# Kernel optimization log

Measured on AMD Instinct MI355X. Metric: run time of the kernel, lower is better.

Reference implementation:

```python
import jax, jax.numpy as jnp
import numpy as np
import math

NEG = -1000000.0


def setup_inputs() -> dict:
    key = jax.random.key(0)
    ks = jax.random.split(key, 8)
    B, S, D = 4, 2048, 1024
    std = 1.0 / math.sqrt(D)
    return {
        "queries": jax.random.normal(ks[0], (B, S, D), jnp.float32),
        "keys": jax.random.normal(ks[1], (B, S, D), jnp.float32),
        "values": jax.random.normal(ks[2], (B, S, D), jnp.float32),
        "valid_len": jax.random.randint(ks[3], (B,), 1, S, dtype=jnp.int64 if jax.config.jax_enable_x64 else jnp.int32),
        "W_q": jax.random.normal(ks[4], (D, D), jnp.float32) * std,
        "W_k": jax.random.normal(ks[5], (D, D), jnp.float32) * std,
        "W_v": jax.random.normal(ks[6], (D, D), jnp.float32) * std,
        "W_o": jax.random.normal(ks[7], (D, D), jnp.float32) * std,
    }


def reference(queries, keys, values, valid_len, W_q, W_k, W_v, W_o):
    NUM_HEADS = 16
    B, S, D = queries.shape
    hd = D // NUM_HEADS

    def split_heads(x):
        # (B, S, D) -> (B, H, S, hd)
        return x.reshape(B, -1, NUM_HEADS, hd).transpose(0, 2, 1, 3)

    # nn.Linear with weight W applies x @ W.T
    q = split_heads(queries @ W_q.T)
    k = split_heads(keys @ W_k.T)
    v = split_heads(values @ W_v.T)

    scale = 1.0 / math.sqrt(hd)
    scores = jnp.einsum('bhqd,bhkd->bhqk', q, k) * scale  # (B, H, Sq, Sk)

    # key-padding mask from valid_len: positions >= valid_len are masked
    kpos = jnp.arange(scores.shape[-1])
    pad_mask = kpos[None, None, None, :] >= valid_len[:, None, None, None]
    scores = jnp.where(pad_mask, NEG, scores)
    attn = jax.nn.softmax(scores, axis=-1)

    out = jnp.einsum('bhqk,bhkd->bhqd', attn, v)  # (B, H, Sq, hd)
    out = out.transpose(0, 2, 1, 3).reshape(B, -1, D)
    return out @ W_o.T
```

## Files before the change

kernel.cpp:

```cpp
#include <hip/hip_runtime.h>
#include <hip/hip_bf16.h>

using bf16_t = __bf16;
using bf16x8 = __attribute__((ext_vector_type(8))) __bf16;
using bf16x4 = __attribute__((ext_vector_type(4))) __bf16;
using f32x4  = __attribute__((ext_vector_type(4))) float;

#define S_  2048
#define D_  1024

typedef __attribute__((address_space(1))) unsigned int glb_u32;
typedef __attribute__((address_space(3))) unsigned int lds_u32;

__device__ __forceinline__ void async_cp16(const void* g, void* lds) {
    __builtin_amdgcn_global_load_lds(
        (glb_u32*)(unsigned long long)g,
        (lds_u32*)(unsigned int)(unsigned long long)lds,
        16, 0, 0);
}

__global__ __launch_bounds__(256) void cast4_f32_bf16(const float* __restrict__ a, const float* __restrict__ b,
                                                      const float* __restrict__ c, const float* __restrict__ dd,
                                                      bf16_t* __restrict__ oa, bf16_t* __restrict__ ob,
                                                      bf16_t* __restrict__ oc, bf16_t* __restrict__ od, int n4) {
    int i = blockIdx.x * 256 + threadIdx.x;
    if (i >= n4) return;
    const float* s; bf16_t* d;
    int w = blockIdx.y;
    if      (w == 0) { s = a;  d = oa; }
    else if (w == 1) { s = b;  d = ob; }
    else if (w == 2) { s = c;  d = oc; }
    else             { s = dd; d = od; }
    float4 f = reinterpret_cast<const float4*>(s)[i];
    bf16x4 o;
    o[0] = (bf16_t)f.x; o[1] = (bf16_t)f.y; o[2] = (bf16_t)f.z; o[3] = (bf16_t)f.w;
    reinterpret_cast<bf16x4*>(d)[i] = o;
}

__global__ __launch_bounds__(256) void cast3_f32_bf16(const float* __restrict__ q, const float* __restrict__ k,
                                                      const float* __restrict__ v,
                                                      bf16_t* __restrict__ oq, bf16_t* __restrict__ ok,
                                                      bf16_t* __restrict__ ov, int n4) {
    int i = blockIdx.x * 256 + threadIdx.x;
    if (i >= n4) return;
    const float* s; bf16_t* d;
    int w = blockIdx.y;
    if      (w == 0) { s = q; d = oq; }
    else if (w == 1) { s = k; d = ok; }
    else             { s = v; d = ov; }
    float4 f = reinterpret_cast<const float4*>(s)[i];
    bf16x4 o;
    o[0] = (bf16_t)f.x; o[1] = (bf16_t)f.y; o[2] = (bf16_t)f.z; o[3] = (bf16_t)f.w;
    reinterpret_cast<bf16x4*>(d)[i] = o;
}

template <int MODE>
__global__ __launch_bounds__(512, 2) void gemm8(const bf16_t* __restrict__ Aq,
                                                const bf16_t* __restrict__ Ak,
                                                const bf16_t* __restrict__ Av,
                                                const bf16_t* __restrict__ Wq,
                                                const bf16_t* __restrict__ Wk,
                                                const bf16_t* __restrict__ Wv,
                                                bf16_t* __restrict__ Qp,
                                                bf16_t* __restrict__ Kp,
                                                bf16_t* __restrict__ Vt,
                                                float cs,
                                                float* __restrict__ Co) {
    __shared__ bf16_t As[2][2][256 * 32];
    __shared__ bf16_t Bs[2][2][256 * 32];
    const int K = 1024;
    constexpr int NKT = 16;
    int tid  = threadIdx.x;
    int lane = tid & 63, w = tid >> 6;
    int l15  = lane & 15, quad = lane >> 4;
    int wr = w >> 2, wc = w & 3;

    int bid = blockIdx.x;
    int xcd = bid & 7, r = bid >> 3;
    int z = 0, r2 = r;
    if (MODE == 0) { z = r >> 4; r2 = r & 15; }
    int m0 = (xcd * 4 + (r2 & 3)) * 256;
    int n0 = (r2 >> 2) * 256;

    const bf16_t *Ag, *Bg;
    if (MODE == 0) {
        Ag = (z == 0) ? Aq : (z == 1) ? Ak : Av;
        Bg = (z == 0) ? Wq : (z == 1) ? Wk : Wv;
    } else { Ag = Aq; Bg = Wq; }

    const bf16_t* aS[2]; const bf16_t* bS[2]; int ldOff[2];
#pragma unroll
    for (int j = 0; j < 2; j++) {
        int c = j * 512 + tid;
        int row = c >> 2, s = c & 3;
        int ks = (s ^ ((row >> 1) & 3)) * 8;
        aS[j] = Ag + (size_t)(m0 + row) * K + ks;
        bS[j] = Bg + (size_t)(n0 + row) * K + ks;
        ldOff[j] = c * 8;
    }
    auto stage = [&](int buf, int t, int half) {
        int kh = half >> 1;
        int koff = t * 64 + kh * 32;
        if ((half & 1) == 0) {
            async_cp16(aS[0] + koff, &As[buf][kh][ldOff[0]]);
            async_cp16(aS[1] + koff, &As[buf][kh][ldOff[1]]);
        } else {
            async_cp16(bS[0] + koff, &Bs[buf][kh][ldOff[0]]);
            async_cp16(bS[1] + koff, &Bs[buf][kh][ldOff[1]]);
        }
    };

    int aoff[8], boff[4];
#pragma unroll
    for (int i = 0; i < 8; i++) {
        int row = wr * 128 + i * 16 + l15;
        aoff[i] = row * 32 + ((quad ^ ((row >> 1) & 3)) * 8);
    }
#pragma unroll
    for (int jn = 0; jn < 4; jn++) {
        int row = wc * 64 + jn * 16 + l15;
        boff[jn] = row * 32 + ((quad ^ ((row >> 1) & 3)) * 8);
    }

    f32x4 acc[8][4] = {};

    stage(0, 0, 0); stage(0, 0, 1); stage(0, 0, 2); stage(0, 0, 3);
    asm volatile("s_waitcnt vmcnt(4)" ::: "memory");
    __builtin_amdgcn_s_barrier();

    for (int t = 0; t < NKT; ++t) {
        int buf = t & 1, nbuf = buf ^ 1;
        bool st = (t + 1 < NKT);
        const bf16_t* A0 = As[buf][0]; const bf16_t* A1 = As[buf][1];
        const bf16_t* B0 = Bs[buf][0]; const bf16_t* B1 = Bs[buf][1];
        bf16x8 af[4], bfr[4];

#pragma unroll
        for (int i = 0; i < 4; i++) af[i] = *reinterpret_cast<const bf16x8*>(&A0[aoff[i]]);
#pragma unroll
        for (int jn = 0; jn < 4; jn++) bfr[jn] = *reinterpret_cast<const bf16x8*>(&B0[boff[jn]]);
        if (st) stage(nbuf, t + 1, 0);
        __builtin_amdgcn_s_barrier();
        asm volatile("s_waitcnt lgkmcnt(0)" ::: "memory");
        __builtin_amdgcn_sched_barrier(0);
        __builtin_amdgcn_s_setprio(1);
#pragma unroll
        for (int i = 0; i < 4; i++)
#pragma unroll
            for (int jn = 0; jn < 4; jn++)
                acc[i][jn] = __builtin_amdgcn_mfma_f32_16x16x32_bf16(af[i], bfr[jn], acc[i][jn], 0, 0, 0);
        __builtin_amdgcn_s_setprio(0);
        __builtin_amdgcn_s_barrier();

#pragma unroll
        for (int i = 0; i < 4; i++) af[i] = *reinterpret_cast<const bf16x8*>(&A0[aoff[4 + i]]);
        if (st) stage(nbuf, t + 1, 1);
        __builtin_amdgcn_s_barrier();
        asm volatile("s_waitcnt lgkmcnt(0)" ::: "memory");
        __builtin_amdgcn_sched_barrier(0);
        __builtin_amdgcn_s_setprio(1);
#pragma unroll
        for (int i = 0; i < 4; i++)
#pragma unroll
            for (int jn = 0; jn < 4; jn++)
                acc[4 + i][jn] = __builtin_amdgcn_mfma_f32_16x16x32_bf16(af[i], bfr[jn], acc[4 + i][jn], 0, 0, 0);
        __builtin_amdgcn_s_setprio(0);
        if (t == NKT - 1) asm volatile("s_waitcnt vmcnt(0)" ::: "memory");
        else              asm volatile("s_waitcnt vmcnt(4)" ::: "memory");
        __builtin_amdgcn_s_barrier();

#pragma unroll
        for (int i = 0; i < 4; i++) af[i] = *reinterpret_cast<const bf16x8*>(&A1[aoff[i]]);
#pragma unroll
        for (int jn = 0; jn < 4; jn++) bfr[jn] = *reinterpret_cast<const bf16x8*>(&B1[boff[jn]]);
        if (st) stage(nbuf, t + 1, 2);
        __builtin_amdgcn_s_barrier();
        asm volatile("s_waitcnt lgkmcnt(0)" ::: "memory");
        __builtin_amdgcn_sched_barrier(0);
        __builtin_amdgcn_s_setprio(1);
#pragma unroll
        for (int i = 0; i < 4; i++)
#pragma unroll
            for (int jn = 0; jn < 4; jn++)
                acc[i][jn] = __builtin_amdgcn_mfma_f32_16x16x32_bf16(af[i], bfr[jn], acc[i][jn], 0, 0, 0);
        __builtin_amdgcn_s_setprio(0);
        __builtin_amdgcn_s_barrier();

#pragma unroll
        for (int i = 0; i < 4; i++) af[i] = *reinterpret_cast<const bf16x8*>(&A1[aoff[4 + i]]);
        if (st) stage(nbuf, t + 1, 3);
        __builtin_amdgcn_s_barrier();
        asm volatile("s_waitcnt lgkmcnt(0)" ::: "memory");
        __builtin_amdgcn_sched_barrier(0);
        __builtin_amdgcn_s_setprio(1);
#pragma unroll
        for (int i = 0; i < 4; i++)
#pragma unroll
            for (int jn = 0; jn < 4; jn++)
                acc[4 + i][jn] = __builtin_amdgcn_mfma_f32_16x16x32_bf16(af[i], bfr[jn], acc[4 + i][jn], 0, 0, 0);
        __builtin_amdgcn_s_setprio(0);
        asm volatile("s_waitcnt vmcnt(4)" ::: "memory");
        __builtin_amdgcn_s_barrier();
    }

    if (MODE == 0 && z == 2) {
#pragma unroll
        for (int i = 0; i < 8; i++)
#pragma unroll
            for (int jn = 0; jn < 4; jn++) {
                int m = m0 + wr * 128 + i * 16 + quad * 4;
                int n = n0 + wc * 64 + jn * 16 + l15;
                bf16x4 o4;
#pragma unroll
                for (int rr = 0; rr < 4; rr++) o4[rr] = (bf16_t)acc[i][jn][rr];
                size_t vrow = (size_t)((m >> 11) * 16 + (n >> 6)) * 64 + (n & 63);
                int ml = m & 2047;
                int mp = (ml & ~31) | (((ml >> 2) & 3) << 3) | (((ml >> 4) & 1) << 2);
                *reinterpret_cast<bf16x4*>(&Vt[vrow * S_ + mp]) = o4;
            }
    } else if (MODE == 0) {
        bf16_t* CoH = (z == 0) ? Qp : Kp;
        float scale = (z == 0) ? cs : 1.0f;
#pragma unroll
        for (int i = 0; i < 8; i++)
#pragma unroll
            for (int jn = 0; jn < 4; jn++)
#pragma unroll
                for (int rr = 0; rr < 4; rr++) {
                    int m = m0 + wr * 128 + i * 16 + quad * 4 + rr;
                    int n = n0 + wc * 64 + jn * 16 + l15;
                    CoH[(size_t)m * 1024 + n] = (bf16_t)(acc[i][jn][rr] * scale);
                }
    } else {
#pragma unroll
        for (int i = 0; i < 8; i++)
#pragma unroll
            for (int jn = 0; jn < 4; jn++)
#pragma unroll
                for (int rr = 0; rr < 4; rr++) {
                    int m = m0 + wr * 128 + i * 16 + quad * 4 + rr;
                    int n = n0 + wc * 64 + jn * 16 + l15;
                    Co[(size_t)m * 1024 + n] = acc[i][jn][rr];
                }
    }
}

__global__ __launch_bounds__(256, 4) void qkv_gemm(const float* __restrict__ qf,
                                                   const float* __restrict__ kf,
                                                   const float* __restrict__ vf,
                                                   const bf16_t* __restrict__ Wqb,
                                                   const bf16_t* __restrict__ Wkb,
                                                   const bf16_t* __restrict__ Wvb,
                                                   bf16_t* __restrict__ Qp,
                                                   bf16_t* __restrict__ Kp,
                                                   bf16_t* __restrict__ Vt,
                                                   float cs) {
    __shared__ bf16_t As[2][128 * 32];
    __shared__ bf16_t Bs[3][128 * 32];
    const int K = 1024;
    int tid  = threadIdx.x;
    int lane = tid & 63;
    int w    = tid >> 6;
    int l15  = lane & 15, quad = lane >> 4;

    int bid = blockIdx.x;
    int xcd = bid & 7, idx = bid >> 3;
    int z   = idx >> 6;
    int rem = idx & 63;
    int m0 = (xcd * 8 + (rem & 7)) * 128;
    int n0 = (rem >> 3) * 128;
    int wm = (w >> 1) * 64, wn = (w & 1) * 64;

    const float*  Af; const bf16_t* Bt;
    if      (z == 0) { Af = qf; Bt = Wqb; }
    else if (z == 1) { Af = kf; Bt = Wkb; }
    else             { Af = vf; Bt = Wvb; }
    float scale = (z == 0) ? cs : 1.0f;

    const float* Ag = Af + (size_t)(m0 + (tid >> 2)) * K + (tid & 3) * 8;
    int arow = tid >> 2, aslot = tid & 3;
    int aoff = arow * 32 + ((aslot ^ ((arow >> 1) & 3)) * 8);

    const bf16_t* bSrc[2]; int bOff[2];
#pragma unroll
    for (int j = 0; j < 2; j++) {
        int linear = j * 256 + tid;
        int row = linear >> 2, s = linear & 3;
        bSrc[j] = Bt + (size_t)(n0 + row) * K + ((s ^ ((row >> 1) & 3)) * 8);
        bOff[j] = linear * 8;
    }

    float4 aE[4], aO[4];
    auto loadA = [&](float4* a, int k0) {
        const float* p = Ag + k0;
        a[0] = *reinterpret_cast<const float4*>(p);
        a[1] = *reinterpret_cast<const float4*>(p + 4);
        a[2] = *reinterpret_cast<const float4*>(p + (size_t)64 * K);
        a[3] = *reinterpret_cast<const float4*>(p + (size_t)64 * K + 4);
    };
    auto storeA = [&](bf16_t* dst, const float4* a) {
        bf16x8 o0, o1;
        o0[0] = (bf16_t)a[0].x; o0[1] = (bf16_t)a[0].y; o0[2] = (bf16_t)a[0].z; o0[3] = (bf16_t)a[0].w;
        o0[4] = (bf16_t)a[1].x; o0[5] = (bf16_t)a[1].y; o0[6] = (bf16_t)a[1].z; o0[7] = (bf16_t)a[1].w;
        o1[0] = (bf16_t)a[2].x; o1[1] = (bf16_t)a[2].y; o1[2] = (bf16_t)a[2].z; o1[3] = (bf16_t)a[2].w;
        o1[4] = (bf16_t)a[3].x; o1[5] = (bf16_t)a[3].y; o1[6] = (bf16_t)a[3].z; o1[7] = (bf16_t)a[3].w;
        *reinterpret_cast<bf16x8*>(dst + aoff)        = o0;
        *reinterpret_cast<bf16x8*>(dst + aoff + 2048) = o1;
    };
    auto stageB = [&](bf16_t* dst, int k0) {
        async_cp16(bSrc[0] + k0, dst + bOff[0]);
        async_cp16(bSrc[1] + k0, dst + bOff[1]);
    };

    f32x4 acc[4][4] = {};
    bf16_t *bRead = Bs[0], *bMid = Bs[1], *bStage = Bs[2];

    loadA(aE, 0);
    stageB(Bs[0], 0);
    loadA(aO, 32);
    stageB(Bs[1], 32);
    storeA(As[0], aE);
    asm volatile("s_waitcnt vmcnt(6) lgkmcnt(0)" ::: "memory");
    __builtin_amdgcn_s_barrier();

#pragma unroll 2
    for (int i = 0; i < 32; ++i) {
        int k2 = (i + 2 < 32) ? (i + 2) * 32 : 992;
        float4* aNew = (i & 1) ? aO : aE;
        loadA(aNew, k2);
        stageB(bStage, k2);

        const bf16_t* Ac = As[i & 1];
        bf16x8 af[4], bfr[4];
#pragma unroll
        for (int t = 0; t < 4; t++) {
            int ra = wm + t * 16 + l15;
            int rb = wn + t * 16 + l15;
            af[t]  = *reinterpret_cast<const bf16x8*>(&Ac[ra * 32 + ((quad ^ ((ra >> 1) & 3)) * 8)]);
            bfr[t] = *reinterpret_cast<const bf16x8*>(&bRead[rb * 32 + ((quad ^ ((rb >> 1) & 3)) * 8)]);
        }
#pragma unroll
        for (int mt = 0; mt < 4; mt++)
#pragma unroll
            for (int nt = 0; nt < 4; nt++)
                acc[mt][nt] = __builtin_amdgcn_mfma_f32_16x16x32_bf16(af[mt], bfr[nt], acc[mt][nt], 0, 0, 0);

        if (i + 1 < 32) storeA(As[(i + 1) & 1], (i & 1) ? aE : aO);

        bf16_t* t0 = bRead; bRead = bMid; bMid = bStage; bStage = t0;
        asm volatile("s_waitcnt vmcnt(6) lgkmcnt(0)" ::: "memory");
        __builtin_amdgcn_s_barrier();
    }

    if (z == 2) {
#pragma unroll
        for (int mt = 0; mt < 4; mt++)
#pragma unroll
            for (int nt = 0; nt < 4; nt++) {
                int m = m0 + wm + mt * 16 + quad * 4;
                int n = n0 + wn + nt * 16 + l15;
                bf16x4 o4;
#pragma unroll
                for (int r = 0; r < 4; r++) o4[r] = (bf16_t)acc[mt][nt][r];
                size_t vrow = (size_t)((m >> 11) * 16 + (n >> 6)) * 64 + (n & 63);
                int ml = m & 2047;
                int mp = (ml & ~31) | (((ml >> 2) & 3) << 3) | (((ml >> 4) & 1) << 2);
                *reinterpret_cast<bf16x4*>(&Vt[vrow * S_ + mp]) = o4;
            }
    } else {
        bf16_t* Co = (z == 0) ? Qp : Kp;
#pragma unroll
        for (int mt = 0; mt < 4; mt++)
#pragma unroll
            for (int nt = 0; nt < 4; nt++)
#pragma unroll
                for (int r = 0; r < 4; r++) {
                    int m = m0 + wm + mt * 16 + quad * 4 + r;
                    int n = n0 + wn + nt * 16 + l15;
                    Co[(size_t)m * 1024 + n] = (bf16_t)(acc[mt][nt][r] * scale);
                }
    }
}

__global__ __launch_bounds__(256) void attn_fused(const bf16_t* __restrict__ Qp,
                                                  const bf16_t* __restrict__ Kp,
                                                  const bf16_t* __restrict__ Vt,
                                                  const int* __restrict__ vlen_p,
                                                  bf16_t* __restrict__ Out) {
    __shared__ bf16_t smem[4][64 * 64];

    int tid  = threadIdx.x;
    int lane = tid & 63, w = tid >> 6;
    int l15  = lane & 15, quad = lane >> 4;

    int nk[4], ord[4] = {0, 1, 2, 3};
#pragma unroll
    for (int i = 0; i < 4; i++) nk[i] = (vlen_p[i] + 63) >> 6;
#pragma unroll
    for (int i = 0; i < 3; i++)
#pragma unroll
        for (int j = 0; j < 3 - i; j++)
            if (nk[ord[j + 1]] > nk[ord[j]]) { int t = ord[j]; ord[j] = ord[j + 1]; ord[j + 1] = t; }

    int bid  = blockIdx.x;
    int b    = ord[bid >> 9];
    int t    = bid & 511;
    int h    = (t & 7) * 2 + ((t >> 3) & 1);
    int qblk = t >> 4;
    int vlen = vlen_p[b];
    int nkb  = (vlen + 63) >> 6;

    const bf16_t* Qg = Qp + (size_t)(b * S_ + qblk * 64) * D_ + h * 64;
    const bf16_t* Kg = Kp + (size_t)b * S_ * D_ + h * 64;
    const bf16_t* Vg = Vt + (size_t)(b * 16 + h) * 64 * S_;

    int r0 = tid >> 3, s0 = tid & 7;
    int sx = (s0 ^ (r0 & 7)) * 8;
    const bf16_t* kS0 = Kg + (size_t)r0 * D_ + sx;
    const bf16_t* kS1 = kS0 + (size_t)32 * D_;
    const bf16_t* vS0 = Vg + (size_t)r0 * S_ + sx;
    const bf16_t* vS1 = vS0 + (size_t)32 * S_;

    {
        const bf16_t* qS0 = Qg + (size_t)r0 * D_ + sx;
        async_cp16(qS0,                   smem[2] + tid * 8);
        async_cp16(qS0 + (size_t)32 * D_, smem[2] + tid * 8 + 2048);
        async_cp16(kS0, smem[0] + tid * 8);
        async_cp16(kS1, smem[0] + tid * 8 + 2048);
        async_cp16(vS0, smem[1] + tid * 8);
        async_cp16(vS1, smem[1] + tid * 8 + 2048);
    }
    __syncthreads();

    bf16x8 qf[2];
    {
        int row = w * 16 + l15, x = row & 7;
#pragma unroll
        for (int kk = 0; kk < 2; kk++)
            qf[kk] = *reinterpret_cast<const bf16x8*>(&smem[2][row * 64 + ((kk * 4 + quad) ^ x) * 8]);
    }
    __syncthreads();

    f32x4 o[4] = {};
    float l_st = 0.f;

    for (int kb = 0; kb < nkb; kb++) {
        int cur = kb & 1;
        if (kb + 1 < nkb) {
            int nxt = cur ^ 1;
            kS0 += (size_t)64 * D_; kS1 += (size_t)64 * D_;
            vS0 += 64;              vS1 += 64;
            async_cp16(kS0, smem[nxt * 2]     + tid * 8);
            async_cp16(kS1, smem[nxt * 2]     + tid * 8 + 2048);
            async_cp16(vS0, smem[nxt * 2 + 1] + tid * 8);
            async_cp16(vS1, smem[nxt * 2 + 1] + tid * 8 + 2048);
        }
        const bf16_t* Kc = smem[cur * 2];
        const bf16_t* Vc = smem[cur * 2 + 1];

        f32x4 sc[4] = {};
#pragma unroll
        for (int nt = 0; nt < 4; nt++) {
            int row = nt * 16 + l15, x = row & 7;
#pragma unroll
            for (int kk = 0; kk < 2; kk++) {
                bf16x8 kf = *reinterpret_cast<const bf16x8*>(&Kc[row * 64 + ((kk * 4 + quad) ^ x) * 8]);
                sc[nt] = __builtin_amdgcn_mfma_f32_16x16x32_bf16(kf, qf[kk], sc[nt], 0, 0, 0);
            }
        }

        bool partial = (vlen & 63) && (kb == nkb - 1);
        bf16x8 pf[2];
        float lacc = 0.f;
        if (!partial) {
#pragma unroll
            for (int nt = 0; nt < 4; nt++)
#pragma unroll
                for (int r = 0; r < 4; r++) {
                    float p = __builtin_exp2f(sc[nt][r]);
                    lacc += p;
                    pf[nt >> 1][(nt & 1) * 4 + r] = (bf16_t)p;
                }
        } else {
#pragma unroll
            for (int nt = 0; nt < 4; nt++)
#pragma unroll
                for (int r = 0; r < 4; r++) {
                    float p = __builtin_exp2f(sc[nt][r]);
                    if (kb * 64 + nt * 16 + quad * 4 + r >= vlen) p = 0.f;
                    lacc += p;
                    pf[nt >> 1][(nt & 1) * 4 + r] = (bf16_t)p;
                }
        }
        l_st += lacc;

#pragma unroll
        for (int np = 0; np < 2; np++)
#pragma unroll
            for (int dt = 0; dt < 4; dt++) {
                int row = dt * 16 + l15, x = row & 7;
                bf16x8 vfr = *reinterpret_cast<const bf16x8*>(&Vc[row * 64 + ((np * 4 + quad) ^ x) * 8]);
                o[dt] = __builtin_amdgcn_mfma_f32_16x16x32_bf16(vfr, pf[np], o[dt], 0, 0, 0);
            }

        __syncthreads();
    }

    float l = l_st;
    l += __shfl_xor(l, 16);
    l += __shfl_xor(l, 32);
    float inv = 1.0f / l;

    bf16_t* T = smem[0];
    {
        int row = w * 16 + l15, x = row & 7;
#pragma unroll
        for (int dt = 0; dt < 4; dt++) {
            bf16x4 o4;
#pragma unroll
            for (int r = 0; r < 4; r++) o4[r] = (bf16_t)(o[dt][r] * inv);
            int slot = dt * 2 + (quad >> 1);
            *reinterpret_cast<bf16x4*>(&T[row * 64 + (slot ^ x) * 8 + (quad & 1) * 4]) = o4;
        }
    }
    __syncthreads();
    {
        int row = tid >> 2, ch = tid & 3, x = row & 7;
        size_t obase = (size_t)(b * S_ + qblk * 64 + row) * D_ + h * 64 + ch * 16;
        bf16x8 f0 = *reinterpret_cast<const bf16x8*>(&T[row * 64 + ((ch * 2)     ^ x) * 8]);
        bf16x8 f1 = *reinterpret_cast<const bf16x8*>(&T[row * 64 + ((ch * 2 + 1) ^ x) * 8]);
        *reinterpret_cast<bf16x8*>(&Out[obase])     = f0;
        *reinterpret_cast<bf16x8*>(&Out[obase + 8]) = f1;
    }
}

__global__ __launch_bounds__(256) void gemm_out(const bf16_t* __restrict__ A,
                                                const bf16_t* __restrict__ Bt,
                                                float* __restrict__ C) {
    __shared__ bf16_t As[3][128 * 32];
    __shared__ bf16_t Bs[3][128 * 32];
    const int K = 1024;
    int tid  = threadIdx.x;
    int lane = tid & 63;
    int w    = tid >> 6;
    int l15  = lane & 15, quad = lane >> 4;

    int bid = blockIdx.x;
    int xcd = bid & 7, idx = bid >> 3;
    int m0 = (xcd * 8 + (idx & 7)) * 128;
    int n0 = (idx >> 3) * 128;
    int wm = (w >> 1) * 64, wn = (w & 1) * 64;

    const bf16_t* aSrc[2]; const bf16_t* bSrc[2];
    int dOff[2];
#pragma unroll
    for (int j = 0; j < 2; j++) {
        int linear = j * 256 + tid;
        int row = linear >> 2, s = linear & 3;
        int sw = (s ^ ((row >> 1) & 3)) * 8;
        aSrc[j] = A  + (size_t)(m0 + row) * K + sw;
        bSrc[j] = Bt + (size_t)(n0 + row) * K + sw;
        dOff[j] = linear * 8;
    }

    auto stage = [&](int buf, int koff) {
#pragma unroll
        for (int j = 0; j < 2; j++) async_cp16(aSrc[j] + koff, &As[buf][dOff[j]]);
#pragma unroll
        for (int j = 0; j < 2; j++) async_cp16(bSrc[j] + koff, &Bs[buf][dOff[j]]);
    };

    f32x4 acc[4][4] = {};

    stage(0, 0);
    stage(1, 32);

    int cur = 0, nx2 = 2;
    for (int i = 0; i < 32; ++i) {
        if (i == 31) asm volatile("s_waitcnt vmcnt(0)" ::: "memory");
        else         asm volatile("s_waitcnt vmcnt(4)" ::: "memory");
        __builtin_amdgcn_s_barrier();
        if (i + 2 < 32) stage(nx2, (i + 2) * 32);

        bf16x8 af[4], bfr[4];
#pragma unroll
        for (int t = 0; t < 4; t++) {
            int ra = wm + t * 16 + l15;
            int rb = wn + t * 16 + l15;
            af[t]  = *reinterpret_cast<const bf16x8*>(&As[cur][ra * 32 + ((quad ^ ((ra >> 1) & 3)) * 8)]);
            bfr[t] = *reinterpret_cast<const bf16x8*>(&Bs[cur][rb * 32 + ((quad ^ ((rb >> 1) & 3)) * 8)]);
        }
#pragma unroll
        for (int mt = 0; mt < 4; mt++)
#pragma unroll
            for (int nt = 0; nt < 4; nt++)
                acc[mt][nt] = __builtin_amdgcn_mfma_f32_16x16x32_bf16(af[mt], bfr[nt], acc[mt][nt], 0, 0, 0);

        cur = (cur == 2) ? 0 : cur + 1;
        nx2 = (nx2 == 2) ? 0 : nx2 + 1;
    }

#pragma unroll
    for (int mt = 0; mt < 4; mt++)
#pragma unroll
        for (int nt = 0; nt < 4; nt++)
#pragma unroll
            for (int r = 0; r < 4; r++) {
                int m = m0 + wm + mt * 16 + quad * 4 + r;
                int n = n0 + wn + nt * 16 + l15;
                C[(size_t)m * 1024 + n] = acc[mt][nt][r];
            }
}

extern "C" void kernel_launch(void* const* d_in, const int* in_sizes, int n_in,
                              void* d_out, int out_size, void* d_ws, size_t ws_size,
                              hipStream_t stream) {
    const float* q  = (const float*)d_in[0];
    const float* k  = (const float*)d_in[1];
    const float* v  = (const float*)d_in[2];
    const int*   vl = (const int*)d_in[3];
    const float* Wq = (const float*)d_in[4];
    const float* Wk = (const float*)d_in[5];
    const float* Wv = (const float*)d_in[6];
    const float* Wo = (const float*)d_in[7];
    float* out = (float*)d_out;

    bf16_t* ws = (bf16_t*)d_ws;
    const size_t SD = (size_t)8192 * 1024;
    const size_t WW = (size_t)1024 * 1024;
    const float cs = 0.18033688f;
    dim3 blk(256);

    size_t need = (6 * SD + 4 * WW) * sizeof(bf16_t);
    if (ws_size >= need) {
        bf16_t* qb  = ws;
        bf16_t* kb  = ws + SD;
        bf16_t* vb  = ws + 2 * SD;
        bf16_t* Qp  = ws + 3 * SD;
        bf16_t* Kp  = ws + 4 * SD;
        bf16_t* Vt  = ws + 5 * SD;
        bf16_t* Wqb = ws + 6 * SD;
        bf16_t* Wkb = Wqb + WW;
        bf16_t* Wvb = Wqb + 2 * WW;
        bf16_t* Wob = Wqb + 3 * WW;

        cast4_f32_bf16<<<dim3(1024, 4), blk, 0, stream>>>(Wq, Wk, Wv, Wo, Wqb, Wkb, Wvb, Wob, 262144);
        cast3_f32_bf16<<<dim3(8192, 3), blk, 0, stream>>>(q, k, v, qb, kb, vb, 2097152);
        gemm8<0><<<dim3(384), dim3(512), 0, stream>>>(qb, kb, vb, Wqb, Wkb, Wvb, Qp, Kp, Vt, cs, nullptr);
        attn_fused<<<dim3(2048), blk, 0, stream>>>(Qp, Kp, Vt, vl, qb);
        gemm8<1><<<dim3(128), dim3(512), 0, stream>>>(qb, nullptr, nullptr, Wob, nullptr, nullptr,
                                                      nullptr, nullptr, nullptr, 1.0f, out);
    } else {
        bf16_t* tmpB = ws + SD;
        bf16_t* Qp   = ws + 2 * SD;
        bf16_t* Kp   = ws + 3 * SD;
        bf16_t* Vt   = ws + 4 * SD;
        bf16_t* Wqb  = ws + 5 * SD;
        bf16_t* Wkb  = Wqb + WW;
        bf16_t* Wvb  = Wqb + 2 * WW;
        bf16_t* Wob  = Wqb + 3 * WW;

        cast4_f32_bf16<<<dim3(1024, 4), blk, 0, stream>>>(Wq, Wk, Wv, Wo, Wqb, Wkb, Wvb, Wob, 262144);
        qkv_gemm<<<dim3(1536), blk, 0, stream>>>(q, k, v, Wqb, Wkb, Wvb, Qp, Kp, Vt, cs);
        attn_fused<<<dim3(2048), blk, 0, stream>>>(Qp, Kp, Vt, vl, tmpB);
        gemm_out<<<dim3(512), blk, 0, stream>>>(tmpB, Wob, out);
    }
}
```

Baseline: 319.9 us.

## Shrink GEMM tile to 128x256 for more blocks; merge cast kernels

```diff
diff --git a/kernel.cpp b/kernel.cpp
--- a/kernel.cpp
+++ b/kernel.cpp
@@ -17,6 +17,31 @@
         (glb_u32*)(unsigned long long)g,
         (lds_u32*)(unsigned int)(unsigned long long)lds,
         16, 0, 0);
+}
+
+__global__ __launch_bounds__(256) void cast7(const float* __restrict__ q, const float* __restrict__ k,
+                                             const float* __restrict__ v, const float* __restrict__ Wq,
+                                             const float* __restrict__ Wk, const float* __restrict__ Wv,
+                                             const float* __restrict__ Wo,
+                                             bf16_t* __restrict__ oq, bf16_t* __restrict__ ok,
+                                             bf16_t* __restrict__ ov, bf16_t* __restrict__ oWq,
+                                             bf16_t* __restrict__ oWk, bf16_t* __restrict__ oWv,
+                                             bf16_t* __restrict__ oWo) {
+    int y = blockIdx.y;
+    int i = blockIdx.x * 256 + threadIdx.x;
+    const float* s; bf16_t* d; int n4;
+    if      (y == 0) { s = q;  d = oq;  n4 = 2097152; }
+    else if (y == 1) { s = k;  d = ok;  n4 = 2097152; }
+    else if (y == 2) { s = v;  d = ov;  n4 = 2097152; }
+    else if (y == 3) { s = Wq; d = oWq; n4 = 262144;  }
+    else if (y == 4) { s = Wk; d = oWk; n4 = 262144;  }
+    else if (y == 5) { s = Wv; d = oWv; n4 = 262144;  }
+    else             { s = Wo; d = oWo; n4 = 262144;  }
+    if (i >= n4) return;
+    float4 f = reinterpret_cast<const float4*>(s)[i];
+    bf16x4 o;
+    o[0] = (bf16_t)f.x; o[1] = (bf16_t)f.y; o[2] = (bf16_t)f.z; o[3] = (bf16_t)f.w;
+    reinterpret_cast<bf16x4*>(d)[i] = o;
 }
 
 __global__ __launch_bounds__(256) void cast4_f32_bf16(const float* __restrict__ a, const float* __restrict__ b,
@@ -37,23 +62,6 @@
     reinterpret_cast<bf16x4*>(d)[i] = o;
 }
 
-__global__ __launch_bounds__(256) void cast3_f32_bf16(const float* __restrict__ q, const float* __restrict__ k,
-                                                      const float* __restrict__ v,
-                                                      bf16_t* __restrict__ oq, bf16_t* __restrict__ ok,
-                                                      bf16_t* __restrict__ ov, int n4) {
-    int i = blockIdx.x * 256 + threadIdx.x;
-    if (i >= n4) return;
-    const float* s; bf16_t* d;
-    int w = blockIdx.y;
-    if      (w == 0) { s = q; d = oq; }
-    else if (w == 1) { s = k; d = ok; }
-    else             { s = v; d = ov; }
-    float4 f = reinterpret_cast<const float4*>(s)[i];
-    bf16x4 o;
-    o[0] = (bf16_t)f.x; o[1] = (bf16_t)f.y; o[2] = (bf16_t)f.z; o[3] = (bf16_t)f.w;
-    reinterpret_cast<bf16x4*>(d)[i] = o;
-}
-
 template <int MODE>
 __global__ __launch_bounds__(512, 2) void gemm8(const bf16_t* __restrict__ Aq,
                                                 const bf16_t* __restrict__ Ak,
@@ -66,7 +74,7 @@
                                                 bf16_t* __restrict__ Vt,
                                                 float cs,
                                                 float* __restrict__ Co) {
-    __shared__ bf16_t As[2][2][256 * 32];
+    __shared__ bf16_t As[2][2][128 * 32];
     __shared__ bf16_t Bs[2][2][256 * 32];
     const int K = 1024;
     constexpr int NKT = 16;
@@ -78,9 +86,9 @@
     int bid = blockIdx.x;
     int xcd = bid & 7, r = bid >> 3;
     int z = 0, r2 = r;
-    if (MODE == 0) { z = r >> 4; r2 = r & 15; }
-    int m0 = (xcd * 4 + (r2 & 3)) * 256;
-    int n0 = (r2 >> 2) * 256;
+    if (MODE == 0) { z = r >> 5; r2 = r & 31; }
+    int m0 = (xcd * 8 + (r2 & 7)) * 128;
+    int n0 = (r2 >> 3) * 256;
 
     const bf16_t *Ag, *Bg;
     if (MODE == 0) {
@@ -88,32 +96,29 @@
         Bg = (z == 0) ? Wq : (z == 1) ? Wk : Wv;
     } else { Ag = Aq; Bg = Wq; }
 
-    const bf16_t* aS[2]; const bf16_t* bS[2]; int ldOff[2];
+    const bf16_t* aS; const bf16_t* bS[2]; int bOff[2];
+    {
+        int row = tid >> 2, s = tid & 3;
+        aS = Ag + (size_t)(m0 + row) * K + ((s ^ ((row >> 1) & 3)) * 8);
+    }
 #pragma unroll
     for (int j = 0; j < 2; j++) {
         int c = j * 512 + tid;
         int row = c >> 2, s = c & 3;
-        int ks = (s ^ ((row >> 1) & 3)) * 8;
-        aS[j] = Ag + (size_t)(m0 + row) * K + ks;
-        bS[j] = Bg + (size_t)(n0 + row) * K + ks;
-        ldOff[j] = c * 8;
-    }
-    auto stage = [&](int buf, int t, int half) {
-        int kh = half >> 1;
+        bS[j] = Bg + (size_t)(n0 + row) * K + ((s ^ ((row >> 1) & 3)) * 8);
+        bOff[j] = c * 8;
+    }
+    auto stage = [&](int buf, int t, int kh) {
         int koff = t * 64 + kh * 32;
-        if ((half & 1) == 0) {
-            async_cp16(aS[0] + koff, &As[buf][kh][ldOff[0]]);
-            async_cp16(aS[1] + koff, &As[buf][kh][ldOff[1]]);
-        } else {
-            async_cp16(bS[0] + koff, &Bs[buf][kh][ldOff[0]]);
-            async_cp16(bS[1] + koff, &Bs[buf][kh][ldOff[1]]);
-        }
+        async_cp16(aS + koff,    &As[buf][kh][tid * 8]);
+        async_cp16(bS[0] + koff, &Bs[buf][kh][bOff[0]]);
+        async_cp16(bS[1] + koff, &Bs[buf][kh][bOff[1]]);
     };
 
-    int aoff[8], boff[4];
-#pragma unroll
-    for (int i = 0; i < 8; i++) {
-        int row = wr * 128 + i * 16 + l15;
+    int aoff[4], boff[4];
+#pragma unroll
+    for (int i = 0; i < 4; i++) {
+        int row = wr * 64 + i * 16 + l15;
         aoff[i] = row * 32 + ((quad ^ ((row >> 1) & 3)) * 8);
     }
 #pragma unroll
@@ -122,93 +127,49 @@
         boff[jn] = row * 32 + ((quad ^ ((row >> 1) & 3)) * 8);
     }
 
-    f32x4 acc[8][4] = {};
-
-    stage(0, 0, 0); stage(0, 0, 1); stage(0, 0, 2); stage(0, 0, 3);
-    asm volatile("s_waitcnt vmcnt(4)" ::: "memory");
+    f32x4 acc[4][4] = {};
+
+    stage(0, 0, 0);
+    stage(0, 0, 1);
+    asm volatile("s_waitcnt vmcnt(3)" ::: "memory");
     __builtin_amdgcn_s_barrier();
 
     for (int t = 0; t < NKT; ++t) {
         int buf = t & 1, nbuf = buf ^ 1;
         bool st = (t + 1 < NKT);
-        const bf16_t* A0 = As[buf][0]; const bf16_t* A1 = As[buf][1];
-        const bf16_t* B0 = Bs[buf][0]; const bf16_t* B1 = Bs[buf][1];
         bf16x8 af[4], bfr[4];
 
 #pragma unroll
-        for (int i = 0; i < 4; i++) af[i] = *reinterpret_cast<const bf16x8*>(&A0[aoff[i]]);
-#pragma unroll
-        for (int jn = 0; jn < 4; jn++) bfr[jn] = *reinterpret_cast<const bf16x8*>(&B0[boff[jn]]);
-        if (st) stage(nbuf, t + 1, 0);
-        __builtin_amdgcn_s_barrier();
-        asm volatile("s_waitcnt lgkmcnt(0)" ::: "memory");
-        __builtin_amdgcn_sched_barrier(0);
-        __builtin_amdgcn_s_setprio(1);
+        for (int kh = 0; kh < 2; kh++) {
+            const bf16_t* Ah = As[buf][kh];
+            const bf16_t* Bh = Bs[buf][kh];
+#pragma unroll
+            for (int i = 0; i < 4; i++)  af[i]  = *reinterpret_cast<const bf16x8*>(&Ah[aoff[i]]);
+#pragma unroll
+            for (int jn = 0; jn < 4; jn++) bfr[jn] = *reinterpret_cast<const bf16x8*>(&Bh[boff[jn]]);
+            if (st) stage(nbuf, t + 1, kh);
+            __builtin_amdgcn_s_barrier();
+            asm volatile("s_waitcnt lgkmcnt(0)" ::: "memory");
+            __builtin_amdgcn_sched_barrier(0);
+            __builtin_amdgcn_s_setprio(1);
+#pragma unroll
+            for (int i = 0; i < 4; i++)
+#pragma unroll
+                for (int jn = 0; jn < 4; jn++)
+                    acc[i][jn] = __builtin_amdgcn_mfma_f32_16x16x32_bf16(af[i], bfr[jn], acc[i][jn], 0, 0, 0);
+            __builtin_amdgcn_s_setprio(0);
+            if (t == NKT - 1) asm volatile("s_waitcnt vmcnt(0)" ::: "memory");
+            else              asm volatile("s_waitcnt vmcnt(3)" ::: "memory");
+            __builtin_amdgcn_s_barrier();
+        }
+    }
+
+    if (MODE == 0 && z == 2) {
 #pragma unroll
         for (int i = 0; i < 4; i++)
 #pragma unroll
-            for (int jn = 0; jn < 4; jn++)
-                acc[i][jn] = __builtin_amdgcn_mfma_f32_16x16x32_bf16(af[i], bfr[jn], acc[i][jn], 0, 0, 0);
-        __builtin_amdgcn_s_setprio(0);
-        __builtin_amdgcn_s_barrier();
-
-#pragma unroll
-        for (int i = 0; i < 4; i++) af[i] = *reinterpret_cast<const bf16x8*>(&A0[aoff[4 + i]]);
-        if (st) stage(nbuf, t + 1, 1);
-        __builtin_amdgcn_s_barrier();
-        asm volatile("s_waitcnt lgkmcnt(0)" ::: "memory");
-        __builtin_amdgcn_sched_barrier(0);
-        __builtin_amdgcn_s_setprio(1);
-#pragma unroll
-        for (int i = 0; i < 4; i++)
-#pragma unroll
-            for (int jn = 0; jn < 4; jn++)
-                acc[4 + i][jn] = __builtin_amdgcn_mfma_f32_16x16x32_bf16(af[i], bfr[jn], acc[4 + i][jn], 0, 0, 0);
-        __builtin_amdgcn_s_setprio(0);
-        if (t == NKT - 1) asm volatile("s_waitcnt vmcnt(0)" ::: "memory");
-        else              asm volatile("s_waitcnt vmcnt(4)" ::: "memory");
-        __builtin_amdgcn_s_barrier();
-
-#pragma unroll
-        for (int i = 0; i < 4; i++) af[i] = *reinterpret_cast<const bf16x8*>(&A1[aoff[i]]);
-#pragma unroll
-        for (int jn = 0; jn < 4; jn++) bfr[jn] = *reinterpret_cast<const bf16x8*>(&B1[boff[jn]]);
-        if (st) stage(nbuf, t + 1, 2);
-        __builtin_amdgcn_s_barrier();
-        asm volatile("s_waitcnt lgkmcnt(0)" ::: "memory");
-        __builtin_amdgcn_sched_barrier(0);
-        __builtin_amdgcn_s_setprio(1);
-#pragma unroll
-        for (int i = 0; i < 4; i++)
-#pragma unroll
-            for (int jn = 0; jn < 4; jn++)
-                acc[i][jn] = __builtin_amdgcn_mfma_f32_16x16x32_bf16(af[i], bfr[jn], acc[i][jn], 0, 0, 0);
-        __builtin_amdgcn_s_setprio(0);
-        __builtin_amdgcn_s_barrier();
-
-#pragma unroll
-        for (int i = 0; i < 4; i++) af[i] = *reinterpret_cast<const bf16x8*>(&A1[aoff[4 + i]]);
-        if (st) stage(nbuf, t + 1, 3);
-        __builtin_amdgcn_s_barrier();
-        asm volatile("s_waitcnt lgkmcnt(0)" ::: "memory");
-        __builtin_amdgcn_sched_barrier(0);
-        __builtin_amdgcn_s_setprio(1);
-#pragma unroll
-        for (int i = 0; i < 4; i++)
-#pragma unroll
-            for (int jn = 0; jn < 4; jn++)
-                acc[4 + i][jn] = __builtin_amdgcn_mfma_f32_16x16x32_bf16(af[i], bfr[jn], acc[4 + i][jn], 0, 0, 0);
-        __builtin_amdgcn_s_setprio(0);
-        asm volatile("s_waitcnt vmcnt(4)" ::: "memory");
-        __builtin_amdgcn_s_barrier();
-    }
-
-    if (MODE == 0 && z == 2) {
-#pragma unroll
-        for (int i = 0; i < 8; i++)
-#pragma unroll
             for (int jn = 0; jn < 4; jn++) {
-                int m = m0 + wr * 128 + i * 16 + quad * 4;
+                int m = m0 + wr * 64 + i * 16 + quad * 4;
                 int n = n0 + wc * 64 + jn * 16 + l15;
                 bf16x4 o4;
 #pragma unroll
@@ -222,23 +183,23 @@
         bf16_t* CoH = (z == 0) ? Qp : Kp;
         float scale = (z == 0) ? cs : 1.0f;
 #pragma unroll
-        for (int i = 0; i < 8; i++)
+        for (int i = 0; i < 4; i++)
 #pragma unroll
             for (int jn = 0; jn < 4; jn++)
 #pragma unroll
                 for (int rr = 0; rr < 4; rr++) {
-                    int m = m0 + wr * 128 + i * 16 + quad * 4 + rr;
+                    int m = m0 + wr * 64 + i * 16 + quad * 4 + rr;
                     int n = n0 + wc * 64 + jn * 16 + l15;
                     CoH[(size_t)m * 1024 + n] = (bf16_t)(acc[i][jn][rr] * scale);
                 }
     } else {
 #pragma unroll
-        for (int i = 0; i < 8; i++)
+        for (int i = 0; i < 4; i++)
 #pragma unroll
             for (int jn = 0; jn < 4; jn++)
 #pragma unroll
                 for (int rr = 0; rr < 4; rr++) {
-                    int m = m0 + wr * 128 + i * 16 + quad * 4 + rr;
+                    int m = m0 + wr * 64 + i * 16 + quad * 4 + rr;
                     int n = n0 + wc * 64 + jn * 16 + l15;
                     Co[(size_t)m * 1024 + n] = acc[i][jn][rr];
                 }
@@ -644,11 +605,11 @@
         bf16_t* Wvb = Wqb + 2 * WW;
         bf16_t* Wob = Wqb + 3 * WW;
 
-        cast4_f32_bf16<<<dim3(1024, 4), blk, 0, stream>>>(Wq, Wk, Wv, Wo, Wqb, Wkb, Wvb, Wob, 262144);
-        cast3_f32_bf16<<<dim3(8192, 3), blk, 0, stream>>>(q, k, v, qb, kb, vb, 2097152);
-        gemm8<0><<<dim3(384), dim3(512), 0, stream>>>(qb, kb, vb, Wqb, Wkb, Wvb, Qp, Kp, Vt, cs, nullptr);
+        cast7<<<dim3(8192, 7), blk, 0, stream>>>(q, k, v, Wq, Wk, Wv, Wo,
+                                                 qb, kb, vb, Wqb, Wkb, Wvb, Wob);
+        gemm8<0><<<dim3(768), dim3(512), 0, stream>>>(qb, kb, vb, Wqb, Wkb, Wvb, Qp, Kp, Vt, cs, nullptr);
         attn_fused<<<dim3(2048), blk, 0, stream>>>(Qp, Kp, Vt, vl, qb);
-        gemm8<1><<<dim3(128), dim3(512), 0, stream>>>(qb, nullptr, nullptr, Wob, nullptr, nullptr,
+        gemm8<1><<<dim3(256), dim3(512), 0, stream>>>(qb, nullptr, nullptr, Wob, nullptr, nullptr,
                                                       nullptr, nullptr, nullptr, 1.0f, out);
     } else {
         bf16_t* tmpB = ws + SD;
```

After: 317.8 us. About the same (-0.7%).
